# Performance work log

Hardware: AMD Instinct MI355X
Metric: run time of the kernel (lower is better)

The kernel has to match this reference:

```python
import jax, jax.numpy as jnp
import numpy as np

D_MODEL = 1024
NUM_HEADS = 16
DEPTH = D_MODEL // NUM_HEADS
B, S = 2, 2048


def setup_inputs() -> dict:
    key = jax.random.key(0)
    ks = jax.random.split(key, 11)
    s = 1.0 / np.sqrt(D_MODEL)
    return {
        "v": jax.random.normal(ks[0], (B, S, D_MODEL), jnp.float32),
        "k": jax.random.normal(ks[1], (B, S, D_MODEL), jnp.float32),
        "q": jax.random.normal(ks[2], (B, S, D_MODEL), jnp.float32),
        "wq": jax.random.normal(ks[3], (D_MODEL, D_MODEL), jnp.float32) * s,
        "bq": jnp.zeros((D_MODEL,), jnp.float32),
        "wk": jax.random.normal(ks[4], (D_MODEL, D_MODEL), jnp.float32) * s,
        "bk": jnp.zeros((D_MODEL,), jnp.float32),
        "wv": jax.random.normal(ks[5], (D_MODEL, D_MODEL), jnp.float32) * s,
        "bv": jnp.zeros((D_MODEL,), jnp.float32),
        "wo": jax.random.normal(ks[6], (D_MODEL, D_MODEL), jnp.float32) * s,
        "bo": jnp.zeros((D_MODEL,), jnp.float32),
    }


def _split_heads(x):
    # [B, S, D] -> [B, H, S, depth]
    b, s, _ = x.shape
    return x.reshape(b, s, NUM_HEADS, DEPTH).transpose(0, 2, 1, 3)


def reference(v, k, q, wq, bq, wk, bk, wv, bv, wo, bo):
    qh = _split_heads(q @ wq + bq)
    kh = _split_heads(k @ wk + bk)
    vh = _split_heads(v @ wv + bv)
    scale = 1.0 / jnp.sqrt(jnp.asarray(DEPTH, jnp.float32))
    logits = jnp.einsum("bhqd,bhkd->bhqk", qh, kh) * scale
    attn = jax.nn.softmax(logits, axis=-1)
    out = jnp.einsum("bhqk,bhkd->bhqd", attn, vh)
    out = out.transpose(0, 2, 1, 3).reshape(q.shape[0], -1, D_MODEL)
    return out @ wo + bo
```

## Files before the change

### kernel.cpp

```cpp
#include <hip/hip_runtime.h>
#include <hip/hip_bf16.h>
#include <math.h>

#define DM   1024
#define SEQ  2048
#define NBAT 2
#define NH   16

typedef __attribute__((ext_vector_type(8)))  short short8;
typedef __attribute__((ext_vector_type(4)))  float f32x4;
typedef __attribute__((ext_vector_type(16))) float f32x16;
typedef unsigned short ushort_t;

__device__ __forceinline__ unsigned short f2bf(float f) {
  unsigned int u = __float_as_uint(f);
  u += 0x7fff + ((u >> 16) & 1);
  return (unsigned short)(u >> 16);
}

__device__ __forceinline__ unsigned cvtpk(float lo, float hi) {
  unsigned r;
  asm("v_cvt_pk_bf16_f32 %0, %1, %2" : "=v"(r) : "v"(lo), "v"(hi));
  return r;
}

__device__ __forceinline__ short8 mk8(unsigned a, unsigned b, unsigned c, unsigned d) {
  union { unsigned u[4]; short8 s; } x;
  x.u[0] = a; x.u[1] = b; x.u[2] = c; x.u[3] = d;
  return x.s;
}

#define GLDS16(g, l)                                                            \
  __builtin_amdgcn_global_load_lds((const __attribute__((address_space(1))) void*)(g), \
                                   (__attribute__((address_space(3))) void*)(l), 16, 0, 0)

__global__ __launch_bounds__(256) void cvt3(const float* __restrict__ q,
                                            const float* __restrict__ k,
                                            const float* __restrict__ v,
                                            ushort_t* __restrict__ qb,
                                            ushort_t* __restrict__ kb,
                                            ushort_t* __restrict__ vb) {
  int z = blockIdx.y;
  const float* s = z == 0 ? q : z == 1 ? k : v;
  ushort_t* d = z == 0 ? qb : z == 1 ? kb : vb;
  int i = (blockIdx.x * 256 + threadIdx.x) * 8;
  f32x4 a = *(const f32x4*)(s + i);
  f32x4 b = *(const f32x4*)(s + i + 4);
  short8 o;
  o[0] = (short)f2bf(a[0]); o[1] = (short)f2bf(a[1]);
  o[2] = (short)f2bf(a[2]); o[3] = (short)f2bf(a[3]);
  o[4] = (short)f2bf(b[0]); o[5] = (short)f2bf(b[1]);
  o[6] = (short)f2bf(b[2]); o[7] = (short)f2bf(b[3]);
  *(short8*)(d + i) = o;
}

__global__ __launch_bounds__(256) void transpose_w4(
    const float* __restrict__ w0, const float* __restrict__ w1,
    const float* __restrict__ w2, const float* __restrict__ w3,
    ushort_t* __restrict__ o0, ushort_t* __restrict__ o1,
    ushort_t* __restrict__ o2, ushort_t* __restrict__ o3) {
  int z = blockIdx.z;
  const float* W = z == 0 ? w0 : z == 1 ? w1 : z == 2 ? w2 : w3;
  ushort_t* Wt = z == 0 ? o0 : z == 1 ? o1 : z == 2 ? o2 : o3;
  __shared__ float tile[32][33];
  int bx = blockIdx.x * 32;
  int by = blockIdx.y * 32;
  int tx = threadIdx.x, ty = threadIdx.y;
#pragma unroll
  for (int i = 0; i < 4; ++i)
    tile[ty + i * 8][tx] = W[(size_t)(by + ty + i * 8) * DM + bx + tx];
  __syncthreads();
#pragma unroll
  for (int i = 0; i < 4; ++i)
    Wt[(size_t)(bx + ty + i * 8) * DM + by + tx] = f2bf(tile[tx][ty + i * 8]);
}

__global__ __launch_bounds__(256) void gemm_qkv(
    const ushort_t* __restrict__ Xq, const ushort_t* __restrict__ Xk, const ushort_t* __restrict__ Xv,
    const ushort_t* __restrict__ Wq, const ushort_t* __restrict__ Wk, const ushort_t* __restrict__ Wv,
    const float* __restrict__ Bq, const float* __restrict__ Bk, const float* __restrict__ Bv,
    ushort_t* __restrict__ Oq, ushort_t* __restrict__ Ok, ushort_t* __restrict__ Ov) {
  const int z = blockIdx.z;
  const ushort_t* X  = z == 0 ? Xq : z == 1 ? Xk : Xv;
  const ushort_t* Wt = z == 0 ? Wq : z == 1 ? Wk : Wv;
  const float* bias  = z == 0 ? Bq : z == 1 ? Bk : Bv;

  __shared__ ushort_t As[128 * 32];
  __shared__ ushort_t Bs[128 * 32];
  const int t = threadIdx.x, l = t & 63, w = t >> 6;
  const int wr = w >> 1, wc = w & 1;
  const int fr = l & 15, fg = l >> 4;
  const int mb = blockIdx.x * 128, nb = blockIdx.y * 128;

  f32x4 acc[4][4] = {};
  const int srow = l >> 2;
  const int scol = (l & 3) * 8;

  for (int kt = 0; kt < DM; kt += 32) {
#pragma unroll
    for (int i = 0; i < 2; ++i) {
      int row = i * 64 + w * 16 + srow;
      GLDS16(X  + (size_t)(mb + row) * DM + kt + scol, &As[i * 2048 + w * 512]);
      GLDS16(Wt + (size_t)(nb + row) * DM + kt + scol, &Bs[i * 2048 + w * 512]);
    }
    __syncthreads();
    short8 af[4], bf[4];
#pragma unroll
    for (int mt = 0; mt < 4; ++mt)
      af[mt] = *(const short8*)&As[(wr * 64 + mt * 16 + fr) * 32 + fg * 8];
#pragma unroll
    for (int nt = 0; nt < 4; ++nt)
      bf[nt] = *(const short8*)&Bs[(wc * 64 + nt * 16 + fr) * 32 + fg * 8];
#pragma unroll
    for (int mt = 0; mt < 4; ++mt)
#pragma unroll
      for (int nt = 0; nt < 4; ++nt)
        acc[mt][nt] = __builtin_amdgcn_mfma_f32_16x16x32_bf16(af[mt], bf[nt], acc[mt][nt], 0, 0, 0);
    __syncthreads();
  }

#pragma unroll
  for (int nt = 0; nt < 4; ++nt) {
    int n = nb + wc * 64 + nt * 16 + fr;
    float bn = bias[n];
#pragma unroll
    for (int mt = 0; mt < 4; ++mt) {
#pragma unroll
      for (int r = 0; r < 4; ++r) {
        int m = mb + wr * 64 + mt * 16 + fg * 4 + r;
        float v = acc[mt][nt][r] + bn;
        if (z == 0) {
          Oq[(size_t)m * DM + n] = f2bf(v * 0.125f);
        } else if (z == 1) {
          Ok[(size_t)m * DM + n] = f2bf(v);
        } else {
          int b = m >> 11, s = m & 2047;
          int h = n >> 6, d = n & 63;
          Ov[(((size_t)(b * NH + h) * 64 + d) * SEQ) + s] = f2bf(v);
        }
      }
    }
  }
}

__global__ __launch_bounds__(256) void gemm_o(const ushort_t* __restrict__ X,
                                              const ushort_t* __restrict__ Wt,
                                              const float* __restrict__ bias,
                                              float* __restrict__ out) {
  __shared__ ushort_t As[128 * 32];
  __shared__ ushort_t Bs[64 * 32];
  const int t = threadIdx.x, l = t & 63, w = t >> 6;
  const int fr = l & 15, fg = l >> 4;
  const int mb = blockIdx.x * 128, nb = blockIdx.y * 64;

  f32x4 acc[2][4] = {};
  const int srow = l >> 2;
  const int scol = (l & 3) * 8;

  for (int kt = 0; kt < DM; kt += 32) {
#pragma unroll
    for (int i = 0; i < 2; ++i) {
      int row = i * 64 + w * 16 + srow;
      GLDS16(X + (size_t)(mb + row) * DM + kt + scol, &As[i * 2048 + w * 512]);
    }
    GLDS16(Wt + (size_t)(nb + w * 16 + srow) * DM + kt + scol, &Bs[w * 512]);
    __syncthreads();
    short8 af[2], bf[4];
#pragma unroll
    for (int mt = 0; mt < 2; ++mt)
      af[mt] = *(const short8*)&As[(w * 32 + mt * 16 + fr) * 32 + fg * 8];
#pragma unroll
    for (int nt = 0; nt < 4; ++nt)
      bf[nt] = *(const short8*)&Bs[(nt * 16 + fr) * 32 + fg * 8];
#pragma unroll
    for (int mt = 0; mt < 2; ++mt)
#pragma unroll
      for (int nt = 0; nt < 4; ++nt)
        acc[mt][nt] = __builtin_amdgcn_mfma_f32_16x16x32_bf16(af[mt], bf[nt], acc[mt][nt], 0, 0, 0);
    __syncthreads();
  }

#pragma unroll
  for (int nt = 0; nt < 4; ++nt) {
    int n = nb + nt * 16 + fr;
    float bn = bias[n];
#pragma unroll
    for (int mt = 0; mt < 2; ++mt)
#pragma unroll
      for (int r = 0; r < 4; ++r) {
        int m = mb + w * 32 + mt * 16 + fg * 4 + r;
        out[(size_t)m * DM + n] = acc[mt][nt][r] + bn;
      }
  }
}

#define KPAD 72
__global__ __launch_bounds__(256) void attn_fwd(const ushort_t* __restrict__ Qh,
                                                const ushort_t* __restrict__ Kh,
                                                const ushort_t* __restrict__ Vt,
                                                ushort_t* __restrict__ Oh) {
  __shared__ ushort_t Ks[64 * KPAD];
  __shared__ ushort_t Vs[64 * KPAD];

  const int t = threadIdx.x, l = t & 63, w = t >> 6;
  const int col = l & 31, hi = l >> 5;
  const int q0 = blockIdx.x * 128;
  const int bh = blockIdx.y;
  const int b = bh >> 4, h = bh & 15;

  const ushort_t* Qp = Qh + (size_t)b * SEQ * DM + h * 64;
  const ushort_t* Kp = Kh + (size_t)b * SEQ * DM + h * 64;
  const ushort_t* Vp = Vt + (size_t)bh * 64 * SEQ;

  const int qrow = q0 + w * 32 + col;
  short8 qf[4];
#pragma unroll
  for (int ds = 0; ds < 4; ++ds)
    qf[ds] = *(const short8*)(Qp + (size_t)qrow * DM + ds * 16 + hi * 8);

  float m_run = -INFINITY, l_run = 0.f;
  f32x16 oA = {}, oB = {};

  const int srow = t >> 3;
  const int scol = (t & 7) * 8;

  short8 k0r = *(const short8*)(Kp + (size_t)srow * DM + scol);
  short8 k1r = *(const short8*)(Kp + (size_t)(32 + srow) * DM + scol);
  short8 v0r = *(const short8*)(Vp + (size_t)srow * SEQ + scol);
  short8 v1r = *(const short8*)(Vp + (size_t)(32 + srow) * SEQ + scol);

  for (int kt = 0; kt < SEQ / 64; ++kt) {
    *(short8*)&Ks[srow * KPAD + scol] = k0r;
    *(short8*)&Ks[(32 + srow) * KPAD + scol] = k1r;
    *(short8*)&Vs[srow * KPAD + scol] = v0r;
    *(short8*)&Vs[(32 + srow) * KPAD + scol] = v1r;
    __syncthreads();

    {
      int kv = (kt + 1) * 64;
      k0r = *(const short8*)(Kp + (size_t)(kv + srow) * DM + scol);
      k1r = *(const short8*)(Kp + (size_t)(kv + 32 + srow) * DM + scol);
      v0r = *(const short8*)(Vp + (size_t)srow * SEQ + kv + scol);
      v1r = *(const short8*)(Vp + (size_t)(32 + srow) * SEQ + kv + scol);
    }

    f32x16 s0 = {}, s1 = {};
#pragma unroll
    for (int ds = 0; ds < 4; ++ds) {
      short8 kf0 = *(const short8*)&Ks[col * KPAD + ds * 16 + hi * 8];
      short8 kf1 = *(const short8*)&Ks[(32 + col) * KPAD + ds * 16 + hi * 8];
      s0 = __builtin_amdgcn_mfma_f32_32x32x16_bf16(kf0, qf[ds], s0, 0, 0, 0);
      s1 = __builtin_amdgcn_mfma_f32_32x32x16_bf16(kf1, qf[ds], s1, 0, 0, 0);
    }

    float mx = s0[0];
#pragma unroll
    for (int r = 1; r < 16; ++r) mx = fmaxf(mx, s0[r]);
#pragma unroll
    for (int r = 0; r < 16; ++r) mx = fmaxf(mx, s1[r]);
    mx = fmaxf(mx, __shfl_xor(mx, 32, 64));

    if (!__all(mx <= m_run + 8.f)) {
      float nm = fmaxf(m_run, mx);
      float alpha = __expf(m_run - nm);
      m_run = nm;
      l_run *= alpha;
#pragma unroll
      for (int r = 0; r < 16; ++r) {
        float a = __shfl(alpha, (r & 3) + 8 * (r >> 2) + 4 * hi, 64);
        oA[r] *= a; oB[r] *= a;
      }
    }

    float rs = 0.f;
    float p0[16], p1[16];
#pragma unroll
    for (int r = 0; r < 16; ++r) { p0[r] = __expf(s0[r] - m_run); rs += p0[r]; }
#pragma unroll
    for (int r = 0; r < 16; ++r) { p1[r] = __expf(s1[r] - m_run); rs += p1[r]; }
    rs += __shfl_xor(rs, 32, 64);
    l_run += rs;

    unsigned wd[16];
#pragma unroll
    for (int i = 0; i < 8; ++i) wd[i] = cvtpk(p0[2 * i], p0[2 * i + 1]);
#pragma unroll
    for (int i = 0; i < 8; ++i) wd[8 + i] = cvtpk(p1[2 * i], p1[2 * i + 1]);
    unsigned rcv[8];
#pragma unroll
    for (int ksub = 0; ksub < 2; ++ksub) {
      int B = ksub * 8, R = ksub * 4;
      rcv[R + 0] = (unsigned)__shfl_xor((int)(hi ? wd[B + 0] : wd[B + 2]), 32, 64);
      rcv[R + 1] = (unsigned)__shfl_xor((int)(hi ? wd[B + 1] : wd[B + 3]), 32, 64);
      rcv[R + 2] = (unsigned)__shfl_xor((int)(hi ? wd[B + 4] : wd[B + 6]), 32, 64);
      rcv[R + 3] = (unsigned)__shfl_xor((int)(hi ? wd[B + 5] : wd[B + 7]), 32, 64);
    }
    short8 pf[4];
#pragma unroll
    for (int ks = 0; ks < 4; ++ks) {
      int B = (ks >> 1) * 8 + (ks & 1) * 4;
      int R = (ks >> 1) * 4 + (ks & 1) * 2;
      unsigned f0 = hi ? rcv[R]     : wd[B];
      unsigned f1 = hi ? rcv[R + 1] : wd[B + 1];
      unsigned f2 = hi ? wd[B + 2]  : rcv[R];
      unsigned f3 = hi ? wd[B + 3]  : rcv[R + 1];
      pf[ks] = mk8(f0, f1, f2, f3);
    }

#pragma unroll
    for (int ks = 0; ks < 4; ++ks) {
      short8 vfA = *(const short8*)&Vs[col * KPAD + ks * 16 + hi * 8];
      short8 vfB = *(const short8*)&Vs[(32 + col) * KPAD + ks * 16 + hi * 8];
      oA = __builtin_amdgcn_mfma_f32_32x32x16_bf16(pf[ks], vfA, oA, 0, 0, 0);
      oB = __builtin_amdgcn_mfma_f32_32x32x16_bf16(pf[ks], vfB, oB, 0, 0, 0);
    }
    __syncthreads();
  }

#pragma unroll
  for (int r = 0; r < 16; ++r) {
    int qr = (r & 3) + 8 * (r >> 2) + 4 * hi;
    float li = __shfl(l_run, qr, 64);
    float inv = __builtin_amdgcn_rcpf(li);
    size_t row = (size_t)(b * SEQ + q0 + w * 32 + qr);
    Oh[row * DM + h * 64 + col]      = f2bf(oA[r] * inv);
    Oh[row * DM + h * 64 + 32 + col] = f2bf(oB[r] * inv);
  }
}

extern "C" void kernel_launch(void* const* d_in, const int* in_sizes, int n_in,
                              void* d_out, int out_size, void* d_ws, size_t ws_size,
                              hipStream_t stream) {
  const float* v  = (const float*)d_in[0];
  const float* k  = (const float*)d_in[1];
  const float* q  = (const float*)d_in[2];
  const float* wq = (const float*)d_in[3];
  const float* bq = (const float*)d_in[4];
  const float* wk = (const float*)d_in[5];
  const float* bk = (const float*)d_in[6];
  const float* wv = (const float*)d_in[7];
  const float* bv = (const float*)d_in[8];
  const float* wo = (const float*)d_in[9];
  const float* bo = (const float*)d_in[10];

  char* ws = (char*)d_ws;
  const size_t MB = 1u << 20;
  ushort_t* qb  = (ushort_t*)(ws + 0 * MB);
  ushort_t* kb  = (ushort_t*)(ws + 8 * MB);
  ushort_t* vb  = (ushort_t*)(ws + 16 * MB);
  ushort_t* wqt = (ushort_t*)(ws + 24 * MB);
  ushort_t* wkt = (ushort_t*)(ws + 26 * MB);
  ushort_t* wvt = (ushort_t*)(ws + 28 * MB);
  ushort_t* wot = (ushort_t*)(ws + 30 * MB);
  ushort_t* Qh  = (ushort_t*)(ws + 32 * MB);
  ushort_t* Kh  = (ushort_t*)(ws + 40 * MB);
  ushort_t* Vt  = (ushort_t*)(ws + 48 * MB);
  ushort_t* AO  = (ushort_t*)(ws + 56 * MB);

  cvt3<<<dim3(2048, 3), 256, 0, stream>>>(q, k, v, qb, kb, vb);
  transpose_w4<<<dim3(32, 32, 4), dim3(32, 8), 0, stream>>>(wq, wk, wv, wo, wqt, wkt, wvt, wot);
  gemm_qkv<<<dim3(32, 8, 3), 256, 0, stream>>>(qb, kb, vb, wqt, wkt, wvt, bq, bk, bv, Qh, Kh, Vt);
  attn_fwd<<<dim3(16, 32), 256, 0, stream>>>(Qh, Kh, Vt, AO);
  gemm_o<<<dim3(32, 16), 256, 0, stream>>>(AO, wot, bo, (float*)d_out);
}
```

Baseline: 236.3 us.

## Merge prep kernels, deepen GEMM K-tiles with swizzle, double-buffer attention, use exp2

```diff
diff --git a/kernel.cpp b/kernel.cpp
--- a/kernel.cpp
+++ b/kernel.cpp
@@ -12,6 +12,9 @@
 typedef __attribute__((ext_vector_type(16))) float f32x16;
 typedef unsigned short ushort_t;
 
+#define QSCALE 0.1803368801111204f
+#define DEFER_THR 11.541560327111708f
+
 __device__ __forceinline__ unsigned short f2bf(float f) {
   unsigned int u = __float_as_uint(f);
   u += 0x7fff + ((u >> 16) & 1);
@@ -34,45 +37,43 @@
   __builtin_amdgcn_global_load_lds((const __attribute__((address_space(1))) void*)(g), \
                                    (__attribute__((address_space(3))) void*)(l), 16, 0, 0)
 
-__global__ __launch_bounds__(256) void cvt3(const float* __restrict__ q,
-                                            const float* __restrict__ k,
-                                            const float* __restrict__ v,
-                                            ushort_t* __restrict__ qb,
-                                            ushort_t* __restrict__ kb,
-                                            ushort_t* __restrict__ vb) {
-  int z = blockIdx.y;
-  const float* s = z == 0 ? q : z == 1 ? k : v;
-  ushort_t* d = z == 0 ? qb : z == 1 ? kb : vb;
-  int i = (blockIdx.x * 256 + threadIdx.x) * 8;
-  f32x4 a = *(const f32x4*)(s + i);
-  f32x4 b = *(const f32x4*)(s + i + 4);
-  short8 o;
-  o[0] = (short)f2bf(a[0]); o[1] = (short)f2bf(a[1]);
-  o[2] = (short)f2bf(a[2]); o[3] = (short)f2bf(a[3]);
-  o[4] = (short)f2bf(b[0]); o[5] = (short)f2bf(b[1]);
-  o[6] = (short)f2bf(b[2]); o[7] = (short)f2bf(b[3]);
-  *(short8*)(d + i) = o;
-}
-
-__global__ __launch_bounds__(256) void transpose_w4(
+__global__ __launch_bounds__(256) void prep(
+    const float* __restrict__ q, const float* __restrict__ k, const float* __restrict__ v,
+    ushort_t* __restrict__ qb, ushort_t* __restrict__ kb, ushort_t* __restrict__ vb,
     const float* __restrict__ w0, const float* __restrict__ w1,
     const float* __restrict__ w2, const float* __restrict__ w3,
     ushort_t* __restrict__ o0, ushort_t* __restrict__ o1,
     ushort_t* __restrict__ o2, ushort_t* __restrict__ o3) {
-  int z = blockIdx.z;
-  const float* W = z == 0 ? w0 : z == 1 ? w1 : z == 2 ? w2 : w3;
-  ushort_t* Wt = z == 0 ? o0 : z == 1 ? o1 : z == 2 ? o2 : o3;
-  __shared__ float tile[32][33];
-  int bx = blockIdx.x * 32;
-  int by = blockIdx.y * 32;
-  int tx = threadIdx.x, ty = threadIdx.y;
-#pragma unroll
-  for (int i = 0; i < 4; ++i)
-    tile[ty + i * 8][tx] = W[(size_t)(by + ty + i * 8) * DM + bx + tx];
-  __syncthreads();
-#pragma unroll
-  for (int i = 0; i < 4; ++i)
-    Wt[(size_t)(bx + ty + i * 8) * DM + by + tx] = f2bf(tile[tx][ty + i * 8]);
+  const int z = blockIdx.y;
+  const int t = threadIdx.x;
+  if (z < 3) {
+    const float* s = z == 0 ? q : z == 1 ? k : v;
+    ushort_t* d = z == 0 ? qb : z == 1 ? kb : vb;
+    int i = (blockIdx.x * 256 + t) * 8;
+    f32x4 a = *(const f32x4*)(s + i);
+    f32x4 b = *(const f32x4*)(s + i + 4);
+    short8 o;
+    o[0] = (short)f2bf(a[0]); o[1] = (short)f2bf(a[1]);
+    o[2] = (short)f2bf(a[2]); o[3] = (short)f2bf(a[3]);
+    o[4] = (short)f2bf(b[0]); o[5] = (short)f2bf(b[1]);
+    o[6] = (short)f2bf(b[2]); o[7] = (short)f2bf(b[3]);
+    *(short8*)(d + i) = o;
+  } else {
+    if (blockIdx.x >= 1024) return;
+    const float* W = z == 3 ? w0 : z == 4 ? w1 : z == 5 ? w2 : w3;
+    ushort_t* Wt = z == 3 ? o0 : z == 4 ? o1 : z == 5 ? o2 : o3;
+    __shared__ float tile[32][33];
+    int bx = (blockIdx.x & 31) * 32;
+    int by = (blockIdx.x >> 5) * 32;
+    int tx = t & 31, ty = t >> 5;
+#pragma unroll
+    for (int i = 0; i < 4; ++i)
+      tile[ty + i * 8][tx] = W[(size_t)(by + ty + i * 8) * DM + bx + tx];
+    __syncthreads();
+#pragma unroll
+    for (int i = 0; i < 4; ++i)
+      Wt[(size_t)(bx + ty + i * 8) * DM + by + tx] = f2bf(tile[tx][ty + i * 8]);
+  }
 }
 
 __global__ __launch_bounds__(256) void gemm_qkv(
@@ -85,37 +86,44 @@
   const ushort_t* Wt = z == 0 ? Wq : z == 1 ? Wk : Wv;
   const float* bias  = z == 0 ? Bq : z == 1 ? Bk : Bv;
 
-  __shared__ ushort_t As[128 * 32];
-  __shared__ ushort_t Bs[128 * 32];
+  __shared__ ushort_t As[128 * 64];
+  __shared__ ushort_t Bs[128 * 64];
   const int t = threadIdx.x, l = t & 63, w = t >> 6;
   const int wr = w >> 1, wc = w & 1;
   const int fr = l & 15, fg = l >> 4;
   const int mb = blockIdx.x * 128, nb = blockIdx.y * 128;
 
   f32x4 acc[4][4] = {};
-  const int srow = l >> 2;
-  const int scol = (l & 3) * 8;
-
-  for (int kt = 0; kt < DM; kt += 32) {
-#pragma unroll
-    for (int i = 0; i < 2; ++i) {
-      int row = i * 64 + w * 16 + srow;
-      GLDS16(X  + (size_t)(mb + row) * DM + kt + scol, &As[i * 2048 + w * 512]);
-      GLDS16(Wt + (size_t)(nb + row) * DM + kt + scol, &Bs[i * 2048 + w * 512]);
-    }
-    __syncthreads();
-    short8 af[4], bf[4];
-#pragma unroll
-    for (int mt = 0; mt < 4; ++mt)
-      af[mt] = *(const short8*)&As[(wr * 64 + mt * 16 + fr) * 32 + fg * 8];
-#pragma unroll
-    for (int nt = 0; nt < 4; ++nt)
-      bf[nt] = *(const short8*)&Bs[(wc * 64 + nt * 16 + fr) * 32 + fg * 8];
-#pragma unroll
-    for (int mt = 0; mt < 4; ++mt)
-#pragma unroll
-      for (int nt = 0; nt < 4; ++nt)
-        acc[mt][nt] = __builtin_amdgcn_mfma_f32_16x16x32_bf16(af[mt], bf[nt], acc[mt][nt], 0, 0, 0);
+  const int srow = w * 8 + (l >> 3);
+  const int gcol = (((l & 7) ^ ((l >> 3) & 7))) * 8;
+
+  for (int kt = 0; kt < DM; kt += 64) {
+#pragma unroll
+    for (int i = 0; i < 4; ++i) {
+      int row = i * 32 + srow;
+      GLDS16(X  + (size_t)(mb + row) * DM + kt + gcol, &As[i * 2048 + w * 512]);
+      GLDS16(Wt + (size_t)(nb + row) * DM + kt + gcol, &Bs[i * 2048 + w * 512]);
+    }
+    __syncthreads();
+#pragma unroll
+    for (int ks = 0; ks < 2; ++ks) {
+      short8 af[4], bf[4];
+#pragma unroll
+      for (int mt = 0; mt < 4; ++mt) {
+        int row = wr * 64 + mt * 16 + fr;
+        af[mt] = *(const short8*)&As[row * 64 + (((ks << 2) | fg) ^ (fr & 7)) * 8];
+      }
+#pragma unroll
+      for (int nt = 0; nt < 4; ++nt) {
+        int row = wc * 64 + nt * 16 + fr;
+        bf[nt] = *(const short8*)&Bs[row * 64 + (((ks << 2) | fg) ^ (fr & 7)) * 8];
+      }
+#pragma unroll
+      for (int mt = 0; mt < 4; ++mt)
+#pragma unroll
+        for (int nt = 0; nt < 4; ++nt)
+          acc[mt][nt] = __builtin_amdgcn_mfma_f32_16x16x32_bf16(af[mt], bf[nt], acc[mt][nt], 0, 0, 0);
+    }
     __syncthreads();
   }
 
@@ -130,7 +138,7 @@
         int m = mb + wr * 64 + mt * 16 + fg * 4 + r;
         float v = acc[mt][nt][r] + bn;
         if (z == 0) {
-          Oq[(size_t)m * DM + n] = f2bf(v * 0.125f);
+          Oq[(size_t)m * DM + n] = f2bf(v * QSCALE);
         } else if (z == 1) {
           Ok[(size_t)m * DM + n] = f2bf(v);
         } else {
@@ -147,36 +155,43 @@
                                               const ushort_t* __restrict__ Wt,
                                               const float* __restrict__ bias,
                                               float* __restrict__ out) {
-  __shared__ ushort_t As[128 * 32];
-  __shared__ ushort_t Bs[64 * 32];
+  __shared__ ushort_t As[128 * 64];
+  __shared__ ushort_t Bs[64 * 64];
   const int t = threadIdx.x, l = t & 63, w = t >> 6;
   const int fr = l & 15, fg = l >> 4;
   const int mb = blockIdx.x * 128, nb = blockIdx.y * 64;
 
   f32x4 acc[2][4] = {};
-  const int srow = l >> 2;
-  const int scol = (l & 3) * 8;
-
-  for (int kt = 0; kt < DM; kt += 32) {
-#pragma unroll
-    for (int i = 0; i < 2; ++i) {
-      int row = i * 64 + w * 16 + srow;
-      GLDS16(X + (size_t)(mb + row) * DM + kt + scol, &As[i * 2048 + w * 512]);
-    }
-    GLDS16(Wt + (size_t)(nb + w * 16 + srow) * DM + kt + scol, &Bs[w * 512]);
-    __syncthreads();
-    short8 af[2], bf[4];
-#pragma unroll
-    for (int mt = 0; mt < 2; ++mt)
-      af[mt] = *(const short8*)&As[(w * 32 + mt * 16 + fr) * 32 + fg * 8];
-#pragma unroll
-    for (int nt = 0; nt < 4; ++nt)
-      bf[nt] = *(const short8*)&Bs[(nt * 16 + fr) * 32 + fg * 8];
-#pragma unroll
-    for (int mt = 0; mt < 2; ++mt)
-#pragma unroll
-      for (int nt = 0; nt < 4; ++nt)
-        acc[mt][nt] = __builtin_amdgcn_mfma_f32_16x16x32_bf16(af[mt], bf[nt], acc[mt][nt], 0, 0, 0);
+  const int srow = w * 8 + (l >> 3);
+  const int gcol = (((l & 7) ^ ((l >> 3) & 7))) * 8;
+
+  for (int kt = 0; kt < DM; kt += 64) {
+#pragma unroll
+    for (int i = 0; i < 4; ++i)
+      GLDS16(X + (size_t)(mb + i * 32 + srow) * DM + kt + gcol, &As[i * 2048 + w * 512]);
+#pragma unroll
+    for (int i = 0; i < 2; ++i)
+      GLDS16(Wt + (size_t)(nb + i * 32 + srow) * DM + kt + gcol, &Bs[i * 2048 + w * 512]);
+    __syncthreads();
+#pragma unroll
+    for (int ks = 0; ks < 2; ++ks) {
+      short8 af[2], bf[4];
+#pragma unroll
+      for (int mt = 0; mt < 2; ++mt) {
+        int row = w * 32 + mt * 16 + fr;
+        af[mt] = *(const short8*)&As[row * 64 + (((ks << 2) | fg) ^ (fr & 7)) * 8];
+      }
+#pragma unroll
+      for (int nt = 0; nt < 4; ++nt) {
+        int row = nt * 16 + fr;
+        bf[nt] = *(const short8*)&Bs[row * 64 + (((ks << 2) | fg) ^ (fr & 7)) * 8];
+      }
+#pragma unroll
+      for (int mt = 0; mt < 2; ++mt)
+#pragma unroll
+        for (int nt = 0; nt < 4; ++nt)
+          acc[mt][nt] = __builtin_amdgcn_mfma_f32_16x16x32_bf16(af[mt], bf[nt], acc[mt][nt], 0, 0, 0);
+    }
     __syncthreads();
   }
 
@@ -195,12 +210,13 @@
 }
 
 #define KPAD 72
+#define KVELEM (64 * KPAD)
 __global__ __launch_bounds__(256) void attn_fwd(const ushort_t* __restrict__ Qh,
                                                 const ushort_t* __restrict__ Kh,
                                                 const ushort_t* __restrict__ Vt,
                                                 ushort_t* __restrict__ Oh) {
-  __shared__ ushort_t Ks[64 * KPAD];
-  __shared__ ushort_t Vs[64 * KPAD];
+  __shared__ ushort_t Ks[2 * KVELEM];
+  __shared__ ushort_t Vs[2 * KVELEM];
 
   const int t = threadIdx.x, l = t & 63, w = t >> 6;
   const int col = l & 31, hi = l >> 5;
@@ -228,30 +244,31 @@
   short8 k1r = *(const short8*)(Kp + (size_t)(32 + srow) * DM + scol);
   short8 v0r = *(const short8*)(Vp + (size_t)srow * SEQ + scol);
   short8 v1r = *(const short8*)(Vp + (size_t)(32 + srow) * SEQ + scol);
-
-  for (int kt = 0; kt < SEQ / 64; ++kt) {
-    *(short8*)&Ks[srow * KPAD + scol] = k0r;
-    *(short8*)&Ks[(32 + srow) * KPAD + scol] = k1r;
-    *(short8*)&Vs[srow * KPAD + scol] = v0r;
-    *(short8*)&Vs[(32 + srow) * KPAD + scol] = v1r;
-    __syncthreads();
-
-    {
-      int kv = (kt + 1) * 64;
-      k0r = *(const short8*)(Kp + (size_t)(kv + srow) * DM + scol);
-      k1r = *(const short8*)(Kp + (size_t)(kv + 32 + srow) * DM + scol);
-      v0r = *(const short8*)(Vp + (size_t)srow * SEQ + kv + scol);
-      v1r = *(const short8*)(Vp + (size_t)(32 + srow) * SEQ + kv + scol);
-    }
+  *(short8*)&Ks[srow * KPAD + scol] = k0r;
+  *(short8*)&Ks[(32 + srow) * KPAD + scol] = k1r;
+  *(short8*)&Vs[srow * KPAD + scol] = v0r;
+  *(short8*)&Vs[(32 + srow) * KPAD + scol] = v1r;
+  k0r = *(const short8*)(Kp + (size_t)(64 + srow) * DM + scol);
+  k1r = *(const short8*)(Kp + (size_t)(96 + srow) * DM + scol);
+  v0r = *(const short8*)(Vp + (size_t)srow * SEQ + 64 + scol);
+  v1r = *(const short8*)(Vp + (size_t)(32 + srow) * SEQ + 64 + scol);
+  __syncthreads();
+
+  const int NT = SEQ / 64;
+  for (int kt = 0; kt < NT; ++kt) {
+    const ushort_t* Kc = &Ks[(kt & 1) * KVELEM];
+    const ushort_t* Vc = &Vs[(kt & 1) * KVELEM];
 
     f32x16 s0 = {}, s1 = {};
+    __builtin_amdgcn_s_setprio(1);
 #pragma unroll
     for (int ds = 0; ds < 4; ++ds) {
-      short8 kf0 = *(const short8*)&Ks[col * KPAD + ds * 16 + hi * 8];
-      short8 kf1 = *(const short8*)&Ks[(32 + col) * KPAD + ds * 16 + hi * 8];
+      short8 kf0 = *(const short8*)&Kc[col * KPAD + ds * 16 + hi * 8];
+      short8 kf1 = *(const short8*)&Kc[(32 + col) * KPAD + ds * 16 + hi * 8];
       s0 = __builtin_amdgcn_mfma_f32_32x32x16_bf16(kf0, qf[ds], s0, 0, 0, 0);
       s1 = __builtin_amdgcn_mfma_f32_32x32x16_bf16(kf1, qf[ds], s1, 0, 0, 0);
     }
+    __builtin_amdgcn_s_setprio(0);
 
     float mx = s0[0];
 #pragma unroll
@@ -260,9 +277,9 @@
     for (int r = 0; r < 16; ++r) mx = fmaxf(mx, s1[r]);
     mx = fmaxf(mx, __shfl_xor(mx, 32, 64));
 
-    if (!__all(mx <= m_run + 8.f)) {
+    if (!__all(mx <= m_run + DEFER_THR)) {
       float nm = fmaxf(m_run, mx);
-      float alpha = __expf(m_run - nm);
+      float alpha = __builtin_amdgcn_exp2f(m_run - nm);
       m_run = nm;
       l_run *= alpha;
 #pragma unroll
@@ -275,9 +292,9 @@
     float rs = 0.f;
     float p0[16], p1[16];
 #pragma unroll
-    for (int r = 0; r < 16; ++r) { p0[r] = __expf(s0[r] - m_run); rs += p0[r]; }
-#pragma unroll
-    for (int r = 0; r < 16; ++r) { p1[r] = __expf(s1[r] - m_run); rs += p1[r]; }
+    for (int r = 0; r < 16; ++r) { p0[r] = __builtin_amdgcn_exp2f(s0[r] - m_run); rs += p0[r]; }
+#pragma unroll
+    for (int r = 0; r < 16; ++r) { p1[r] = __builtin_amdgcn_exp2f(s1[r] - m_run); rs += p1[r]; }
     rs += __shfl_xor(rs, 32, 64);
     l_run += rs;
 
@@ -307,14 +324,30 @@
       pf[ks] = mk8(f0, f1, f2, f3);
     }
 
+    __builtin_amdgcn_s_setprio(1);
 #pragma unroll
     for (int ks = 0; ks < 4; ++ks) {
-      short8 vfA = *(const short8*)&Vs[col * KPAD + ks * 16 + hi * 8];
-      short8 vfB = *(const short8*)&Vs[(32 + col) * KPAD + ks * 16 + hi * 8];
+      short8 vfA = *(const short8*)&Vc[col * KPAD + ks * 16 + hi * 8];
+      short8 vfB = *(const short8*)&Vc[(32 + col) * KPAD + ks * 16 + hi * 8];
       oA = __builtin_amdgcn_mfma_f32_32x32x16_bf16(pf[ks], vfA, oA, 0, 0, 0);
       oB = __builtin_amdgcn_mfma_f32_32x32x16_bf16(pf[ks], vfB, oB, 0, 0, 0);
     }
-    __syncthreads();
+    __builtin_amdgcn_s_setprio(0);
+
+    if (kt + 1 < NT) {
+      ushort_t* Kn = &Ks[((kt + 1) & 1) * KVELEM];
+      ushort_t* Vn = &Vs[((kt + 1) & 1) * KVELEM];
+      *(short8*)&Kn[srow * KPAD + scol] = k0r;
+      *(short8*)&Kn[(32 + srow) * KPAD + scol] = k1r;
+      *(short8*)&Vn[srow * KPAD + scol] = v0r;
+      *(short8*)&Vn[(32 + srow) * KPAD + scol] = v1r;
+      int kv2 = (kt + 2 < NT) ? (kt + 2) * 64 : 0;
+      k0r = *(const short8*)(Kp + (size_t)(kv2 + srow) * DM + scol);
+      k1r = *(const short8*)(Kp + (size_t)(kv2 + 32 + srow) * DM + scol);
+      v0r = *(const short8*)(Vp + (size_t)srow * SEQ + kv2 + scol);
+      v1r = *(const short8*)(Vp + (size_t)(32 + srow) * SEQ + kv2 + scol);
+      __syncthreads();
+    }
   }
 
 #pragma unroll
@@ -357,8 +390,8 @@
   ushort_t* Vt  = (ushort_t*)(ws + 48 * MB);
   ushort_t* AO  = (ushort_t*)(ws + 56 * MB);
 
-  cvt3<<<dim3(2048, 3), 256, 0, stream>>>(q, k, v, qb, kb, vb);
-  transpose_w4<<<dim3(32, 32, 4), dim3(32, 8), 0, stream>>>(wq, wk, wv, wo, wqt, wkt, wvt, wot);
+  prep<<<dim3(2048, 7), 256, 0, stream>>>(q, k, v, qb, kb, vb,
+                                          wq, wk, wv, wo, wqt, wkt, wvt, wot);
   gemm_qkv<<<dim3(32, 8, 3), 256, 0, stream>>>(qb, kb, vb, wqt, wkt, wvt, bq, bk, bv, Qh, Kh, Vt);
   attn_fwd<<<dim3(16, 32), 256, 0, stream>>>(Qh, Kh, Vt, AO);
   gemm_o<<<dim3(32, 16), 256, 0, stream>>>(AO, wot, bo, (float*)d_out);
```

New measurement: 231.2 us. -2.1%, faster.
